# Kernel tuning notes

Hardware: AMD Instinct MI355X
Metric: run time of the kernel (lower is better)

The kernel has to match this reference:

```python
import jax, jax.numpy as jnp
import numpy as np

FIELDS = 32
EMBED = 64
PAIRS = FIELDS * (FIELDS - 1) // 2  # 496
BATCH = 2048


def setup_inputs() -> dict:
    key = jax.random.key(0)
    k1, k2 = jax.random.split(key)
    x = jax.random.normal(k1, (BATCH, FIELDS, EMBED), dtype=jnp.float32)
    kernel = jax.random.normal(k2, (EMBED, PAIRS, EMBED), dtype=jnp.float32) * 0.05
    return {"x": x, "kernel": kernel}


def reference(x, kernel):
    # Pair enumeration (i<j) matching the python double loop order.
    iu, ju = jnp.triu_indices(FIELDS, k=1)
    p = x[:, iu, :]  # (B, P, E)
    q = x[:, ju, :]  # (B, P, E)
    # Original: kp[b,f,pr] = sum_e p[b,pr,e]*kernel[f,pr,e];
    # result[b,pr] = sum_f kp[b,f,pr]*q[b,pr,f]
    # => bilinear form per pair, fused as a single einsum.
    result = jnp.einsum('bpe,fpe,bpf->bp', p, kernel, q)
    return result
```

## Files before the change

### kernel.cpp

```cpp
#include <hip/hip_runtime.h>


constexpr int BATCH  = 2048;
constexpr int FIELDS = 32;
constexpr int EMBED  = 64;
constexpr int PAIRS  = FIELDS * (FIELDS - 1) / 2;

typedef __attribute__((ext_vector_type(8))) short  short8;
typedef __attribute__((ext_vector_type(4))) float  f32x4;

constexpr size_t XN      = (size_t)BATCH * FIELDS * EMBED;
constexpr size_t KPN     = (size_t)PAIRS * 2 * 4 * 64 * 8;
constexpr size_t XH_OFF  = 0;
constexpr size_t XL_OFF  = XH_OFF + XN * 2;
constexpr size_t KPH_OFF = XL_OFF + XN * 2;
constexpr size_t KPL_OFF = KPH_OFF + KPN * 2;
constexpr size_t WS_NEED = KPL_OFF + KPN * 2;

constexpr int XSPLIT_BLOCKS = (int)(XN / 4 / 256);
constexpr int KPACK_BLOCKS  = (int)(PAIRS * 512 / 256);

__device__ __forceinline__ unsigned short bf16_rne(float f) {
    unsigned int u = __float_as_uint(f);
    u = u + 0x7fffu + ((u >> 16) & 1u);
    return (unsigned short)(u >> 16);
}

__global__ __launch_bounds__(256) void prep_kernel(
    const float* __restrict__ x,
    const float* __restrict__ kern,
    unsigned short* __restrict__ xh,
    unsigned short* __restrict__ xl,
    unsigned short* __restrict__ kph,
    unsigned short* __restrict__ kpl)
{
    const int bid = (int)blockIdx.x;
    const int tid = (int)threadIdx.x;

    if (bid < XSPLIT_BLOCKS) {
        const int idx = bid * 256 + tid;
        const float4 v = ((const float4*)x)[idx];
        const float vv[4] = {v.x, v.y, v.z, v.w};
        unsigned short h[4], l[4];
        #pragma unroll
        for (int j = 0; j < 4; ++j) {
            const unsigned int u = __float_as_uint(vv[j]);
            h[j] = (unsigned short)(u >> 16);
            l[j] = bf16_rne(vv[j] - __uint_as_float(u & 0xffff0000u));
        }
        ((ushort4*)xh)[idx] = make_ushort4(h[0], h[1], h[2], h[3]);
        ((ushort4*)xl)[idx] = make_ushort4(l[0], l[1], l[2], l[3]);
    } else {
        const int t    = (bid - XSPLIT_BLOCKS) * 256 + tid;
        const int lane = t & 63;
        const int nc   = (t >> 6) & 3;
        const int ks   = (t >> 8) & 1;
        const int pair = t >> 9;
        const int e    = nc * 16 + (lane & 15);
        const int f0   = ks * 32 + (lane >> 4) * 8;

        short8 h8, l8;
        #pragma unroll
        for (int jj = 0; jj < 8; ++jj) {
            const float v = kern[((size_t)(f0 + jj) * PAIRS + pair) * EMBED + e];
            const unsigned int u = __float_as_uint(v);
            h8[jj] = (short)(u >> 16);
            l8[jj] = (short)bf16_rne(v - __uint_as_float(u & 0xffff0000u));
        }
        *(short8*)(kph + (size_t)t * 8) = h8;
        *(short8*)(kpl + (size_t)t * 8) = l8;
    }
}

__global__ __launch_bounds__(256, 3) void opn_mfma_kernel(
    const float* __restrict__ x,
    const unsigned short* __restrict__ xh,
    const unsigned short* __restrict__ xl,
    const unsigned short* __restrict__ kph,
    const unsigned short* __restrict__ kpl,
    float* __restrict__ out)
{
    const int bid  = (int)blockIdx.x;
    const int p    = bid % PAIRS;
    const int mt   = bid / PAIRS;
    const int wave = (int)threadIdx.x >> 6;
    const int lane = (int)threadIdx.x & 63;
    const int Mb   = mt * 128 + wave * 32;
    const int g    = lane >> 4;
    const int c    = lane & 15;

    int i = 0, rem = p;
    while (rem >= FIELDS - 1 - i) { rem -= FIELDS - 1 - i; ++i; }
    const int jf = i + 1 + rem;

    f32x4 acc[2][4];
    #pragma unroll
    for (int mr = 0; mr < 2; ++mr)
        #pragma unroll
        for (int nc = 0; nc < 4; ++nc)
            acc[mr][nc] = (f32x4){0.f, 0.f, 0.f, 0.f};

    #pragma unroll
    for (int ks = 0; ks < 2; ++ks) {
        short8 ah[2], al[2];
        #pragma unroll
        for (int mr = 0; mr < 2; ++mr) {
            const int row = Mb + mr * 16 + c;
            const size_t off = ((size_t)row * FIELDS + jf) * EMBED + ks * 32 + g * 8;
            ah[mr] = *(const short8*)(xh + off);
            al[mr] = *(const short8*)(xl + off);
        }
        short8 bh[4], bl[4];
        #pragma unroll
        for (int nc = 0; nc < 4; ++nc) {
            const size_t kidx = (((size_t)(p * 2 + ks) * 4 + nc) * 64 + lane) * 8;
            bh[nc] = *(const short8*)(kph + kidx);
            bl[nc] = *(const short8*)(kpl + kidx);
        }
        #pragma unroll
        for (int mr = 0; mr < 2; ++mr)
            #pragma unroll
            for (int nc = 0; nc < 4; ++nc) {
                acc[mr][nc] = __builtin_amdgcn_mfma_f32_16x16x32_bf16(ah[mr], bh[nc], acc[mr][nc], 0, 0, 0);
                acc[mr][nc] = __builtin_amdgcn_mfma_f32_16x16x32_bf16(ah[mr], bl[nc], acc[mr][nc], 0, 0, 0);
                acc[mr][nc] = __builtin_amdgcn_mfma_f32_16x16x32_bf16(al[mr], bh[nc], acc[mr][nc], 0, 0, 0);
            }
    }

    float z[2][4];
    #pragma unroll
    for (int mr = 0; mr < 2; ++mr)
        #pragma unroll
        for (int t = 0; t < 4; ++t)
            z[mr][t] = 0.f;

    const size_t xi_base = (size_t)i * EMBED + c;
    #pragma unroll
    for (int mr = 0; mr < 2; ++mr)
        #pragma unroll
        for (int t = 0; t < 4; ++t) {
            const int row = Mb + mr * 16 + 4 * g + t;
            const float* xi = x + (size_t)row * (FIELDS * EMBED) + xi_base;
            #pragma unroll
            for (int nc = 0; nc < 4; ++nc)
                z[mr][t] = fmaf(acc[mr][nc][t], xi[nc * 16], z[mr][t]);
        }

    #pragma unroll
    for (int mask = 1; mask < 16; mask <<= 1)
        #pragma unroll
        for (int mr = 0; mr < 2; ++mr)
            #pragma unroll
            for (int t = 0; t < 4; ++t)
                z[mr][t] += __shfl_xor(z[mr][t], mask, 64);

    if (c < 4) {
        const int t = c;
        #pragma unroll
        for (int mr = 0; mr < 2; ++mr) {
            const int row = Mb + mr * 16 + 4 * g + t;
            out[(size_t)row * PAIRS + p] = z[mr][t];
        }
    }
}

__global__ __launch_bounds__(64) void opn_fp32_kernel(
    const float* __restrict__ x,
    const float* __restrict__ kern,
    float* __restrict__ out)
{
    const int bid   = (int)blockIdx.x;
    const int p     = bid >> 5;
    const int btile = bid & 31;
    const int lane  = (int)threadIdx.x;
    const int b     = btile * 64 + lane;

    int i = 0, rem = p;
    while (rem >= FIELDS - 1 - i) { rem -= FIELDS - 1 - i; ++i; }
    const int j = i + 1 + rem;

    const float* xrow_i = x + (size_t)b * (FIELDS * EMBED) + i * EMBED;
    const float* xrow_j = x + (size_t)b * (FIELDS * EMBED) + j * EMBED;
    const float* kp     = kern + (size_t)p * EMBED;

    float acc[EMBED];
    #pragma unroll
    for (int e = 0; e < EMBED; ++e) acc[e] = 0.0f;

    const float4* xj4 = (const float4*)xrow_j;
    #pragma unroll 2
    for (int f4 = 0; f4 < EMBED / 4; ++f4) {
        const float4 v = xj4[f4];
        const float xjf[4] = {v.x, v.y, v.z, v.w};
        #pragma unroll
        for (int s = 0; s < 4; ++s) {
            const float* kf = kp + (size_t)(f4 * 4 + s) * (PAIRS * EMBED);
            #pragma unroll
            for (int e = 0; e < EMBED; ++e)
                acc[e] = fmaf(xjf[s], kf[e], acc[e]);
        }
    }

    float r = 0.0f;
    const float4* xi4 = (const float4*)xrow_i;
    #pragma unroll
    for (int e4 = 0; e4 < EMBED / 4; ++e4) {
        const float4 u = xi4[e4];
        r = fmaf(u.x, acc[e4 * 4 + 0], r);
        r = fmaf(u.y, acc[e4 * 4 + 1], r);
        r = fmaf(u.z, acc[e4 * 4 + 2], r);
        r = fmaf(u.w, acc[e4 * 4 + 3], r);
    }
    out[(size_t)b * PAIRS + p] = r;
}

extern "C" void kernel_launch(void* const* d_in, const int* in_sizes, int n_in,
                              void* d_out, int out_size, void* d_ws, size_t ws_size,
                              hipStream_t stream) {
    const float* x    = (const float*)d_in[0];
    const float* kern = (const float*)d_in[1];
    float*       out  = (float*)d_out;

    if (ws_size < WS_NEED) {
        opn_fp32_kernel<<<dim3(PAIRS * 32), dim3(64), 0, stream>>>(x, kern, out);
        return;
    }

    char* ws = (char*)d_ws;
    unsigned short* xhi = (unsigned short*)(ws + XH_OFF);
    unsigned short* xlo = (unsigned short*)(ws + XL_OFF);
    unsigned short* kph = (unsigned short*)(ws + KPH_OFF);
    unsigned short* kpl = (unsigned short*)(ws + KPL_OFF);

    prep_kernel<<<dim3(XSPLIT_BLOCKS + KPACK_BLOCKS), dim3(256), 0, stream>>>(
        x, kern, xhi, xlo, kph, kpl);
    opn_mfma_kernel<<<dim3(PAIRS * 16), dim3(256), 0, stream>>>(
        x, xhi, xlo, kph, kpl, out);
}
```

Baseline: 132.7 us.

## Keep per-pair kernel fragments in registers and loop over batch tiles per block

The MFMA kernel now launches one block per pair. Each block loads that pair's packed kernel fragments into registers once and loops over 16 batch tiles, instead of reloading them in every batch-tile block. The mathematical roles are swapped: x_i is the MFMA A operand and x_j is used in the epilogue, so the kernel pack now indexes kernel[f,p,e] contiguously over e and can use float4 loads in prep. Occupancy hint drops to 2 waves per SIMD to hold the extra registers. The grid shrinks to 496 blocks, which may underfill the GPU's CUs and serializes 16 tiles per block.

```diff
diff --git a/kernel.cpp b/kernel.cpp
--- a/kernel.cpp
+++ b/kernel.cpp
@@ -56,23 +56,27 @@
         const int nc   = (t >> 6) & 3;
         const int ks   = (t >> 8) & 1;
         const int pair = t >> 9;
-        const int e    = nc * 16 + (lane & 15);
-        const int f0   = ks * 32 + (lane >> 4) * 8;
+        const int f    = nc * 16 + (lane & 15);
+        const int e0   = ks * 32 + (lane >> 4) * 8;
+
+        const float* src = kern + ((size_t)f * PAIRS + pair) * EMBED + e0;
+        const float4 v0 = *(const float4*)(src);
+        const float4 v1 = *(const float4*)(src + 4);
+        const float vv[8] = {v0.x, v0.y, v0.z, v0.w, v1.x, v1.y, v1.z, v1.w};
 
         short8 h8, l8;
         #pragma unroll
         for (int jj = 0; jj < 8; ++jj) {
-            const float v = kern[((size_t)(f0 + jj) * PAIRS + pair) * EMBED + e];
-            const unsigned int u = __float_as_uint(v);
+            const unsigned int u = __float_as_uint(vv[jj]);
             h8[jj] = (short)(u >> 16);
-            l8[jj] = (short)bf16_rne(v - __uint_as_float(u & 0xffff0000u));
+            l8[jj] = (short)bf16_rne(vv[jj] - __uint_as_float(u & 0xffff0000u));
         }
         *(short8*)(kph + (size_t)t * 8) = h8;
         *(short8*)(kpl + (size_t)t * 8) = l8;
     }
 }
 
-__global__ __launch_bounds__(256, 3) void opn_mfma_kernel(
+__global__ __launch_bounds__(256, 2) void opn_mfma_kernel(
     const float* __restrict__ x,
     const unsigned short* __restrict__ xh,
     const unsigned short* __restrict__ xl,
@@ -80,12 +84,9 @@
     const unsigned short* __restrict__ kpl,
     float* __restrict__ out)
 {
-    const int bid  = (int)blockIdx.x;
-    const int p    = bid % PAIRS;
-    const int mt   = bid / PAIRS;
+    const int p    = (int)blockIdx.x;
     const int wave = (int)threadIdx.x >> 6;
     const int lane = (int)threadIdx.x & 63;
-    const int Mb   = mt * 128 + wave * 32;
     const int g    = lane >> 4;
     const int c    = lane & 15;
 
@@ -93,73 +94,83 @@
     while (rem >= FIELDS - 1 - i) { rem -= FIELDS - 1 - i; ++i; }
     const int jf = i + 1 + rem;
 
-    f32x4 acc[2][4];
+    short8 bh[2][4], bl[2][4];
     #pragma unroll
-    for (int mr = 0; mr < 2; ++mr)
-        #pragma unroll
-        for (int nc = 0; nc < 4; ++nc)
-            acc[mr][nc] = (f32x4){0.f, 0.f, 0.f, 0.f};
-
-    #pragma unroll
-    for (int ks = 0; ks < 2; ++ks) {
-        short8 ah[2], al[2];
+    for (int ks = 0; ks < 2; ++ks)
+        #pragma unroll
+        for (int nc = 0; nc < 4; ++nc) {
+            const size_t kidx = (((size_t)(p * 2 + ks) * 4 + nc) * 64 + lane) * 8;
+            bh[ks][nc] = *(const short8*)(kph + kidx);
+            bl[ks][nc] = *(const short8*)(kpl + kidx);
+        }
+
+    for (int it = 0; it < 16; ++it) {
+        const int Mb = it * 128 + wave * 32;
+
+        short8 ah[2][2], al[2][2];
         #pragma unroll
         for (int mr = 0; mr < 2; ++mr) {
             const int row = Mb + mr * 16 + c;
-            const size_t off = ((size_t)row * FIELDS + jf) * EMBED + ks * 32 + g * 8;
-            ah[mr] = *(const short8*)(xh + off);
-            al[mr] = *(const short8*)(xl + off);
-        }
-        short8 bh[4], bl[4];
-        #pragma unroll
-        for (int nc = 0; nc < 4; ++nc) {
-            const size_t kidx = (((size_t)(p * 2 + ks) * 4 + nc) * 64 + lane) * 8;
-            bh[nc] = *(const short8*)(kph + kidx);
-            bl[nc] = *(const short8*)(kpl + kidx);
-        }
+            const size_t off0 = ((size_t)row * FIELDS + i) * EMBED + g * 8;
+            #pragma unroll
+            for (int ks = 0; ks < 2; ++ks) {
+                ah[mr][ks] = *(const short8*)(xh + off0 + ks * 32);
+                al[mr][ks] = *(const short8*)(xl + off0 + ks * 32);
+            }
+        }
+
+        f32x4 acc[2][4];
         #pragma unroll
         for (int mr = 0; mr < 2; ++mr)
             #pragma unroll
-            for (int nc = 0; nc < 4; ++nc) {
-                acc[mr][nc] = __builtin_amdgcn_mfma_f32_16x16x32_bf16(ah[mr], bh[nc], acc[mr][nc], 0, 0, 0);
-                acc[mr][nc] = __builtin_amdgcn_mfma_f32_16x16x32_bf16(ah[mr], bl[nc], acc[mr][nc], 0, 0, 0);
-                acc[mr][nc] = __builtin_amdgcn_mfma_f32_16x16x32_bf16(al[mr], bh[nc], acc[mr][nc], 0, 0, 0);
+            for (int nc = 0; nc < 4; ++nc)
+                acc[mr][nc] = (f32x4){0.f, 0.f, 0.f, 0.f};
+
+        #pragma unroll
+        for (int ks = 0; ks < 2; ++ks)
+            #pragma unroll
+            for (int mr = 0; mr < 2; ++mr)
+                #pragma unroll
+                for (int nc = 0; nc < 4; ++nc) {
+                    acc[mr][nc] = __builtin_amdgcn_mfma_f32_16x16x32_bf16(ah[mr][ks], bh[ks][nc], acc[mr][nc], 0, 0, 0);
+                    acc[mr][nc] = __builtin_amdgcn_mfma_f32_16x16x32_bf16(ah[mr][ks], bl[ks][nc], acc[mr][nc], 0, 0, 0);
+                    acc[mr][nc] = __builtin_amdgcn_mfma_f32_16x16x32_bf16(al[mr][ks], bh[ks][nc], acc[mr][nc], 0, 0, 0);
+                }
+
+        float z[2][4];
+        #pragma unroll
+        for (int mr = 0; mr < 2; ++mr)
+            #pragma unroll
+            for (int t = 0; t < 4; ++t)
+                z[mr][t] = 0.f;
+
+        const size_t xj_base = (size_t)jf * EMBED + c;
+        #pragma unroll
+        for (int mr = 0; mr < 2; ++mr)
+            #pragma unroll
+            for (int t = 0; t < 4; ++t) {
+                const int row = Mb + mr * 16 + 4 * g + t;
+                const float* xj = x + (size_t)row * (FIELDS * EMBED) + xj_base;
+                #pragma unroll
+                for (int nc = 0; nc < 4; ++nc)
+                    z[mr][t] = fmaf(acc[mr][nc][t], xj[nc * 16], z[mr][t]);
             }
-    }
-
-    float z[2][4];
-    #pragma unroll
-    for (int mr = 0; mr < 2; ++mr)
-        #pragma unroll
-        for (int t = 0; t < 4; ++t)
-            z[mr][t] = 0.f;
-
-    const size_t xi_base = (size_t)i * EMBED + c;
-    #pragma unroll
-    for (int mr = 0; mr < 2; ++mr)
-        #pragma unroll
-        for (int t = 0; t < 4; ++t) {
-            const int row = Mb + mr * 16 + 4 * g + t;
-            const float* xi = x + (size_t)row * (FIELDS * EMBED) + xi_base;
-            #pragma unroll
-            for (int nc = 0; nc < 4; ++nc)
-                z[mr][t] = fmaf(acc[mr][nc][t], xi[nc * 16], z[mr][t]);
-        }
-
-    #pragma unroll
-    for (int mask = 1; mask < 16; mask <<= 1)
-        #pragma unroll
-        for (int mr = 0; mr < 2; ++mr)
-            #pragma unroll
-            for (int t = 0; t < 4; ++t)
-                z[mr][t] += __shfl_xor(z[mr][t], mask, 64);
-
-    if (c < 4) {
-        const int t = c;
-        #pragma unroll
-        for (int mr = 0; mr < 2; ++mr) {
-            const int row = Mb + mr * 16 + 4 * g + t;
-            out[(size_t)row * PAIRS + p] = z[mr][t];
+
+        #pragma unroll
+        for (int mask = 1; mask < 16; mask <<= 1)
+            #pragma unroll
+            for (int mr = 0; mr < 2; ++mr)
+                #pragma unroll
+                for (int t = 0; t < 4; ++t)
+                    z[mr][t] += __shfl_xor(z[mr][t], mask, 64);
+
+        if (c < 4) {
+            const int t = c;
+            #pragma unroll
+            for (int mr = 0; mr < 2; ++mr) {
+                const int row = Mb + mr * 16 + 4 * g + t;
+                out[(size_t)row * PAIRS + p] = z[mr][t];
+            }
         }
     }
 }
@@ -234,6 +245,6 @@
 
     prep_kernel<<<dim3(XSPLIT_BLOCKS + KPACK_BLOCKS), dim3(256), 0, stream>>>(
         x, kern, xhi, xlo, kph, kpl);
-    opn_mfma_kernel<<<dim3(PAIRS * 16), dim3(256), 0, stream>>>(
+    opn_mfma_kernel<<<dim3(PAIRS), dim3(256), 0, stream>>>(
         x, xhi, xlo, kph, kpl, out);
 }
```

After: 129.4 us. 1.03x faster.
